# Kernel optimization log

Hardware: AMD Instinct MI355X
Metric: run time of the kernel (lower is better)

Reference implementation:

```python
import jax, jax.numpy as jnp
import numpy as np

B, H = 64, 1024
K_CONV = 4


def setup_inputs() -> dict:
    key = jax.random.key(0)
    ks = jax.random.split(key, 12)

    def lin(k, i, o, w_scale=None, b_init=None):
        k1, k2 = jax.random.split(k)
        w = jax.random.normal(k1, (i, o), jnp.float32) / np.float32(np.sqrt(i))
        if b_init is None:
            b = jnp.zeros((o,), jnp.float32)
        else:
            b = b_init(k2, o)
        return w, b

    Wq, bq = lin(ks[0], H, H)
    Wk, bk = lin(ks[1], H, H)
    Wv, bv = lin(ks[2], H, H)
    # qk_conv: Conv(in_features=1, out_features=1, kernel_size=4) -> kernel (4,1,1), bias (1,)
    conv_w = jax.random.normal(ks[3], (K_CONV, 1, 1), jnp.float32) * 0.5
    conv_b = jnp.zeros((1,), jnp.float32)
    Wi, bi = lin(ks[4], H, 1, b_init=lambda k, o: jax.random.normal(k, (o,), jnp.float32) * 0.01)
    Wf, bf = lin(ks[5], H, 1, b_init=lambda k, o: jax.random.uniform(k, (o,), jnp.float32, 3.0, 6.0))
    Wo, bo = lin(ks[6], H, H)
    Wskip, bskip = lin(ks[7], H, H)

    c = jnp.zeros((B * H * H,), jnp.float32)
    n = jnp.zeros((B * H,), jnp.float32)
    m = jnp.zeros((B,), jnp.float32)
    x = jax.random.normal(ks[8], (B, H), jnp.float32)

    return {
        "c": c, "n": n, "m": m, "x": x,
        "Wq": Wq, "bq": bq, "Wk": Wk, "bk": bk, "Wv": Wv, "bv": bv,
        "conv_w": conv_w, "conv_b": conv_b,
        "Wi": Wi, "bi": bi, "Wf": Wf, "bf": bf,
        "Wo": Wo, "bo": bo, "Wskip": Wskip, "bskip": bskip,
    }


def reference(c, n, m, x, Wq, bq, Wk, bk, Wv, bv, conv_w, conv_b,
              Wi, bi, Wf, bf, Wo, bo, Wskip, bskip):
    cell = c.reshape(-1, H, H)        # (b, h, h)
    norm = n.reshape(-1, H)           # (b, h)

    out = jax.nn.sigmoid(x @ Wo + bo)                 # (b, h)
    i_tilde = jnp.squeeze(x @ Wi + bi, axis=1)        # (b,)
    f_tilde = jnp.squeeze(x @ Wf + bf, axis=1)        # (b,)

    m_new = jnp.maximum(f_tilde + m, i_tilde)
    i_g = jnp.exp(i_tilde - m_new)
    f_g = jnp.exp(f_tilde + m - m_new)

    # depthwise-style 1D conv over feature axis, 1 in / 1 out channel, SAME pad
    qk = jax.lax.conv_general_dilated(
        x[..., None], conv_w, window_strides=(1,), padding='SAME',
        dimension_numbers=('NWC', 'WIO', 'NWC')) + conv_b   # (b, h, 1)
    qk = jax.nn.silu(qk)[..., 0]                            # (b, h)

    key_ = (qk @ Wk + bk) / jnp.sqrt(jnp.float32(H))  # (b, h)
    query = qk @ Wq + bq                              # (b, h)
    value = x @ Wv + bv                               # (b, h)

    # gated outer-product memory update
    c_new = f_g[:, None, None] * cell + i_g[:, None, None] * (value[:, :, None] * key_[:, None, :])
    n_new = f_g[:, None] * norm + i_g[:, None] * key_

    scaler = jnp.abs(jnp.einsum('bi,bi->b', n_new, query))
    scaler = 1.0 / jnp.maximum(scaler, 1.0)
    h = out * (jnp.einsum('bik,bk->bi', c_new, query) * scaler[:, None])
    h = h + qk @ Wskip + bskip

    return (c_new.reshape(-1), n_new.reshape(-1), m_new, h)
```

## Files before the change

### kernel.cpp

```cpp
#include <hip/hip_runtime.h>
#include <cmath>

#define HH 1024
#define BB 64

#define C_ELEMS ((size_t)BB * HH * HH)

typedef float f4 __attribute__((ext_vector_type(4)));

__device__ __forceinline__ float sigm(float v) { return 1.0f / (1.0f + expf(-v)); }

__global__ __launch_bounds__(256) void kA(
    const float* __restrict__ x, const float* __restrict__ m,
    const float* __restrict__ cw, const float* __restrict__ cb,
    const float* __restrict__ Wi, const float* __restrict__ bi,
    const float* __restrict__ Wf, const float* __restrict__ bf,
    float* __restrict__ qk, float* __restrict__ ig,
    float* __restrict__ fg, float* __restrict__ m_out)
{
    int b = blockIdx.x;
    int tid = threadIdx.x;
    const float* xb = x + (size_t)b * HH;
    float w0 = cw[0], w1 = cw[1], w2 = cw[2], w3 = cw[3], cbv = cb[0];
    int j4 = tid * 4;
    float4 xv = *(const float4*)&xb[j4];
    float xm1 = (tid > 0) ? xb[j4 - 1] : 0.f;
    float xp4 = (tid < 255) ? xb[j4 + 4] : 0.f;
    float xp5 = (tid < 255) ? xb[j4 + 5] : 0.f;
    float s0 = cbv + w0 * xm1  + w1 * xv.x + w2 * xv.y + w3 * xv.z;
    float s1 = cbv + w0 * xv.x + w1 * xv.y + w2 * xv.z + w3 * xv.w;
    float s2 = cbv + w0 * xv.y + w1 * xv.z + w2 * xv.w + w3 * xp4;
    float s3 = cbv + w0 * xv.z + w1 * xv.w + w2 * xp4  + w3 * xp5;
    float4 q;
    q.x = s0 * sigm(s0); q.y = s1 * sigm(s1);
    q.z = s2 * sigm(s2); q.w = s3 * sigm(s3);
    *(float4*)&qk[(size_t)b * HH + j4] = q;

    float4 wi4 = *(const float4*)&Wi[j4];
    float4 wf4 = *(const float4*)&Wf[j4];
    float pi = xv.x * wi4.x + xv.y * wi4.y + xv.z * wi4.z + xv.w * wi4.w;
    float pf = xv.x * wf4.x + xv.y * wf4.y + xv.z * wf4.z + xv.w * wf4.w;

    #pragma unroll
    for (int o = 32; o > 0; o >>= 1) {
        pi += __shfl_down(pi, o, 64);
        pf += __shfl_down(pf, o, 64);
    }
    __shared__ float ri[4], rf[4];
    int wid = tid >> 6, lane = tid & 63;
    if (lane == 0) { ri[wid] = pi; rf[wid] = pf; }
    __syncthreads();
    if (tid == 0) {
        float it = ri[0] + ri[1] + ri[2] + ri[3] + bi[0];
        float ft = rf[0] + rf[1] + rf[2] + rf[3] + bf[0];
        float mo = m[b];
        float mn = fmaxf(ft + mo, it);
        m_out[b] = mn;
        ig[b] = expf(it - mn);
        fg[b] = expf(ft + mo - mn);
    }
}

__global__ __launch_bounds__(256) void kB(
    const float* __restrict__ x, const float* __restrict__ qk,
    const float* __restrict__ Wo, const float* __restrict__ Wv,
    const float* __restrict__ Wk, const float* __restrict__ Wq,
    const float* __restrict__ Wsk, float* __restrict__ part)
{
    int jt = blockIdx.x, ks = blockIdx.y, mat = blockIdx.z;
    const float* W; const float* src;
    switch (mat) {
        case 0: W = Wo;  src = x;  break;
        case 1: W = Wv;  src = x;  break;
        case 2: W = Wk;  src = qk; break;
        case 3: W = Wq;  src = qk; break;
        default: W = Wsk; src = qk; break;
    }
    int j0 = jt * 64;
    int i_base = ks * 128;
    int tid = threadIdx.x;
    int jg = tid & 15;
    int bg = tid >> 4;
    int b0 = bg * 4;

    __shared__ float wlds[32 * 64];
    __shared__ float xlds[32 * 68];

    float acc[4][4];
    #pragma unroll
    for (int a = 0; a < 4; ++a)
        #pragma unroll
        for (int d = 0; d < 4; ++d) acc[a][d] = 0.f;

    for (int ch = 0; ch < 4; ++ch) {
        int i0 = i_base + ch * 32;
        {
            int ii = tid >> 4;
            int c4 = (tid & 15) * 4;
            float4 wa = *(const float4*)&W[(size_t)(i0 + ii) * HH + j0 + c4];
            float4 wb = *(const float4*)&W[(size_t)(i0 + ii + 16) * HH + j0 + c4];
            *(float4*)&wlds[ii * 64 + c4] = wa;
            *(float4*)&wlds[(ii + 16) * 64 + c4] = wb;
        }
        {
            int b = tid >> 2;
            int ii0 = (tid & 3) * 8;
            float4 xa = *(const float4*)&src[(size_t)b * HH + i0 + ii0];
            float4 xb = *(const float4*)&src[(size_t)b * HH + i0 + ii0 + 4];
            xlds[(ii0 + 0) * 68 + b] = xa.x;
            xlds[(ii0 + 1) * 68 + b] = xa.y;
            xlds[(ii0 + 2) * 68 + b] = xa.z;
            xlds[(ii0 + 3) * 68 + b] = xa.w;
            xlds[(ii0 + 4) * 68 + b] = xb.x;
            xlds[(ii0 + 5) * 68 + b] = xb.y;
            xlds[(ii0 + 6) * 68 + b] = xb.z;
            xlds[(ii0 + 7) * 68 + b] = xb.w;
        }
        __syncthreads();
        #pragma unroll
        for (int ii = 0; ii < 32; ++ii) {
            float4 wv = *(const float4*)&wlds[ii * 64 + jg * 4];
            float4 xv = *(const float4*)&xlds[ii * 68 + b0];
            acc[0][0] += xv.x * wv.x; acc[0][1] += xv.x * wv.y;
            acc[0][2] += xv.x * wv.z; acc[0][3] += xv.x * wv.w;
            acc[1][0] += xv.y * wv.x; acc[1][1] += xv.y * wv.y;
            acc[1][2] += xv.y * wv.z; acc[1][3] += xv.y * wv.w;
            acc[2][0] += xv.z * wv.x; acc[2][1] += xv.z * wv.y;
            acc[2][2] += xv.z * wv.z; acc[2][3] += xv.z * wv.w;
            acc[3][0] += xv.w * wv.x; acc[3][1] += xv.w * wv.y;
            acc[3][2] += xv.w * wv.z; acc[3][3] += xv.w * wv.w;
        }
        __syncthreads();
    }
    float* p = part + (size_t)(mat * 8 + ks) * (BB * HH);
    #pragma unroll
    for (int a = 0; a < 4; ++a) {
        float4 v = make_float4(acc[a][0], acc[a][1], acc[a][2], acc[a][3]);
        *(float4*)&p[(size_t)(b0 + a) * HH + j0 + jg * 4] = v;
    }
}

__global__ __launch_bounds__(256) void kC(
    const float* __restrict__ part, const float* __restrict__ n_in,
    const float* __restrict__ bo, const float* __restrict__ bv,
    const float* __restrict__ bk, const float* __restrict__ bq,
    const float* __restrict__ bsk,
    const float* __restrict__ ig, const float* __restrict__ fg,
    float* __restrict__ out_s, float* __restrict__ value_s,
    float* __restrict__ key_s, float* __restrict__ query_s,
    float* __restrict__ skip_s, float* __restrict__ dotp,
    float* __restrict__ n_out)
{
    int seg = blockIdx.x, b = blockIdx.y;
    int tid = threadIdx.x;
    int j = seg * 256 + tid;
    size_t base = (size_t)b * HH + j;
    float s0 = 0.f, s1 = 0.f, s2 = 0.f, s3 = 0.f, s4 = 0.f;
    #pragma unroll
    for (int ksp = 0; ksp < 8; ++ksp) {
        size_t o = (size_t)ksp * (BB * HH) + base;
        s0 += part[(size_t)(0 * 8) * (BB * HH) + o];
        s1 += part[(size_t)(1 * 8) * (BB * HH) + o];
        s2 += part[(size_t)(2 * 8) * (BB * HH) + o];
        s3 += part[(size_t)(3 * 8) * (BB * HH) + o];
        s4 += part[(size_t)(4 * 8) * (BB * HH) + o];
    }
    const float rsH = 0.03125f;
    float og = sigm(s0 + bo[j]);
    float vl = s1 + bv[j];
    float ky = (s2 + bk[j]) * rsH;
    float qu = s3 + bq[j];
    float sk = s4 + bsk[j];

    out_s[base]   = og;
    value_s[base] = vl;
    key_s[base]   = ky;
    query_s[base] = qu;
    skip_s[base]  = sk;

    float igv = ig[b], fgv = fg[b];
    float nn = fgv * n_in[base] + igv * ky;
    n_out[base] = nn;

    float d = nn * qu;
    #pragma unroll
    for (int o = 32; o > 0; o >>= 1) d += __shfl_down(d, o, 64);
    __shared__ float red[4];
    int wid = tid >> 6, lane = tid & 63;
    if (lane == 0) red[wid] = d;
    __syncthreads();
    if (tid == 0) dotp[b * 4 + seg] = red[0] + red[1] + red[2] + red[3];
}

__global__ __launch_bounds__(256) void kD(
    const float* __restrict__ c,
    const float* __restrict__ key_s, const float* __restrict__ query_s,
    const float* __restrict__ value_s, const float* __restrict__ out_s,
    const float* __restrict__ skip_s, const float* __restrict__ ig,
    const float* __restrict__ fg, const float* __restrict__ dotp,
    float* __restrict__ c_out, float* __restrict__ h_out)
{
    int wid = threadIdx.x >> 6;
    int lane = threadIdx.x & 63;
    int r = blockIdx.x * 4 + wid;
    int b = r >> 10;
    float fgv = fg[b];
    float iv = ig[b] * value_s[r];
    const f4* crow = (const f4*)(c + ((size_t)r << 10));
    f4* orow = (f4*)(c_out + ((size_t)r << 10));
    const float* keyb = key_s + (size_t)b * HH;
    const float* qb = query_s + (size_t)b * HH;
    float dot = 0.f;
    #pragma unroll
    for (int kk = 0; kk < 4; ++kk) {
        int k4 = kk * 64 + lane;
        f4 c4 = __builtin_nontemporal_load(&crow[k4]);
        float4 kx = *(const float4*)&keyb[k4 * 4];
        float4 q4 = *(const float4*)&qb[k4 * 4];
        f4 cn;
        cn.x = fgv * c4.x + iv * kx.x;
        cn.y = fgv * c4.y + iv * kx.y;
        cn.z = fgv * c4.z + iv * kx.z;
        cn.w = fgv * c4.w + iv * kx.w;
        __builtin_nontemporal_store(cn, &orow[k4]);
        dot += cn.x * q4.x + cn.y * q4.y + cn.z * q4.z + cn.w * q4.w;
    }
    #pragma unroll
    for (int d = 32; d > 0; d >>= 1) dot += __shfl_down(dot, d, 64);
    if (lane == 0) {
        float ds = dotp[b * 4 + 0] + dotp[b * 4 + 1] + dotp[b * 4 + 2] + dotp[b * 4 + 3];
        float scl = 1.0f / fmaxf(fabsf(ds), 1.0f);
        h_out[r] = out_s[r] * dot * scl + skip_s[r];
    }
}

extern "C" void kernel_launch(void* const* d_in, const int* in_sizes, int n_in,
                              void* d_out, int out_size, void* d_ws, size_t ws_size,
                              hipStream_t stream)
{
    const float* c   = (const float*)d_in[0];
    const float* n   = (const float*)d_in[1];
    const float* m   = (const float*)d_in[2];
    const float* x   = (const float*)d_in[3];
    const float* Wq  = (const float*)d_in[4];
    const float* bq  = (const float*)d_in[5];
    const float* Wk  = (const float*)d_in[6];
    const float* bk  = (const float*)d_in[7];
    const float* Wv  = (const float*)d_in[8];
    const float* bv  = (const float*)d_in[9];
    const float* cw  = (const float*)d_in[10];
    const float* cb  = (const float*)d_in[11];
    const float* Wi  = (const float*)d_in[12];
    const float* bi  = (const float*)d_in[13];
    const float* Wf  = (const float*)d_in[14];
    const float* bf  = (const float*)d_in[15];
    const float* Wo  = (const float*)d_in[16];
    const float* bo  = (const float*)d_in[17];
    const float* Wsk = (const float*)d_in[18];
    const float* bsk = (const float*)d_in[19];

    float* out = (float*)d_out;
    float* ws  = (float*)d_ws;

    const int BH = BB * HH;
    float* qk      = ws;
    float* ig      = ws + BH;
    float* fg      = ig + BB;
    float* dotp    = fg + BB;
    float* fin     = dotp + 256;
    float* out_s   = fin + 0 * BH;
    float* value_s = fin + 1 * BH;
    float* key_s   = fin + 2 * BH;
    float* query_s = fin + 3 * BH;
    float* skip_s  = fin + 4 * BH;
    float* part    = fin + 5 * BH;

    float* c_out = out;
    float* n_out = out + C_ELEMS;
    float* m_out = out + C_ELEMS + BH;
    float* h_out = m_out + BB;

    kA<<<BB, 256, 0, stream>>>(x, m, cw, cb, Wi, bi, Wf, bf, qk, ig, fg, m_out);
    dim3 gB(16, 8, 5);
    kB<<<gB, 256, 0, stream>>>(x, qk, Wo, Wv, Wk, Wq, Wsk, part);
    dim3 gC(4, BB);
    kC<<<gC, 256, 0, stream>>>(part, n, bo, bv, bk, bq, bsk, ig, fg,
                               out_s, value_s, key_s, query_s, skip_s, dotp, n_out);
    kD<<<BH / 4, 256, 0, stream>>>(c, key_s, query_s, value_s, out_s, skip_s,
                                   ig, fg, dotp, c_out, h_out);
}
```

Baseline: 477.8 us.

## Fuse split-K reduction epilogue into GEMV kernel via last-block atomic counter

Removes the separate reduction kernel kC by having the last of the 40 blocks that finish each 64-column tile, detected through an atomic counter reset in kA, sum the split-K partials and compute the gates, key, query, value, skip, n_new and per-tile dot partials. Per-batch dot partials are now stored 16 per batch and summed with vector loads in kD. This saves one kernel launch and its scheduling gap, at the cost of threadfence and atomic overhead and a serialized tail in the finishing block of each tile. The dominant cost is still kD streaming the large c matrix, so the saving is small relative to total time.

```diff
diff --git a/kernel.cpp b/kernel.cpp
--- a/kernel.cpp
+++ b/kernel.cpp
@@ -16,10 +16,12 @@
     const float* __restrict__ Wi, const float* __restrict__ bi,
     const float* __restrict__ Wf, const float* __restrict__ bf,
     float* __restrict__ qk, float* __restrict__ ig,
-    float* __restrict__ fg, float* __restrict__ m_out)
+    float* __restrict__ fg, float* __restrict__ m_out,
+    unsigned* __restrict__ cnt)
 {
     int b = blockIdx.x;
     int tid = threadIdx.x;
+    if (b == 0 && tid < 16) cnt[tid] = 0u;
     const float* xb = x + (size_t)b * HH;
     float w0 = cw[0], w1 = cw[1], w2 = cw[2], w3 = cw[3], cbv = cb[0];
     int j4 = tid * 4;
@@ -65,7 +67,16 @@
     const float* __restrict__ x, const float* __restrict__ qk,
     const float* __restrict__ Wo, const float* __restrict__ Wv,
     const float* __restrict__ Wk, const float* __restrict__ Wq,
-    const float* __restrict__ Wsk, float* __restrict__ part)
+    const float* __restrict__ Wsk, float* __restrict__ part,
+    const float* __restrict__ n_in,
+    const float* __restrict__ bo, const float* __restrict__ bv,
+    const float* __restrict__ bk, const float* __restrict__ bq,
+    const float* __restrict__ bsk,
+    const float* __restrict__ ig, const float* __restrict__ fg,
+    float* __restrict__ out_s, float* __restrict__ value_s,
+    float* __restrict__ key_s, float* __restrict__ query_s,
+    float* __restrict__ skip_s, float* __restrict__ dotp,
+    float* __restrict__ n_out, unsigned* __restrict__ cnt)
 {
     int jt = blockIdx.x, ks = blockIdx.y, mat = blockIdx.z;
     const float* W; const float* src;
@@ -85,6 +96,7 @@
 
     __shared__ float wlds[32 * 64];
     __shared__ float xlds[32 * 68];
+    __shared__ unsigned old_s;
 
     float acc[4][4];
     #pragma unroll
@@ -138,58 +150,62 @@
         float4 v = make_float4(acc[a][0], acc[a][1], acc[a][2], acc[a][3]);
         *(float4*)&p[(size_t)(b0 + a) * HH + j0 + jg * 4] = v;
     }
-}
-
-__global__ __launch_bounds__(256) void kC(
-    const float* __restrict__ part, const float* __restrict__ n_in,
-    const float* __restrict__ bo, const float* __restrict__ bv,
-    const float* __restrict__ bk, const float* __restrict__ bq,
-    const float* __restrict__ bsk,
-    const float* __restrict__ ig, const float* __restrict__ fg,
-    float* __restrict__ out_s, float* __restrict__ value_s,
-    float* __restrict__ key_s, float* __restrict__ query_s,
-    float* __restrict__ skip_s, float* __restrict__ dotp,
-    float* __restrict__ n_out)
-{
-    int seg = blockIdx.x, b = blockIdx.y;
-    int tid = threadIdx.x;
-    int j = seg * 256 + tid;
-    size_t base = (size_t)b * HH + j;
-    float s0 = 0.f, s1 = 0.f, s2 = 0.f, s3 = 0.f, s4 = 0.f;
-    #pragma unroll
-    for (int ksp = 0; ksp < 8; ++ksp) {
-        size_t o = (size_t)ksp * (BB * HH) + base;
-        s0 += part[(size_t)(0 * 8) * (BB * HH) + o];
-        s1 += part[(size_t)(1 * 8) * (BB * HH) + o];
-        s2 += part[(size_t)(2 * 8) * (BB * HH) + o];
-        s3 += part[(size_t)(3 * 8) * (BB * HH) + o];
-        s4 += part[(size_t)(4 * 8) * (BB * HH) + o];
-    }
-    const float rsH = 0.03125f;
-    float og = sigm(s0 + bo[j]);
-    float vl = s1 + bv[j];
-    float ky = (s2 + bk[j]) * rsH;
-    float qu = s3 + bq[j];
-    float sk = s4 + bsk[j];
-
-    out_s[base]   = og;
-    value_s[base] = vl;
-    key_s[base]   = ky;
-    query_s[base] = qu;
-    skip_s[base]  = sk;
-
-    float igv = ig[b], fgv = fg[b];
-    float nn = fgv * n_in[base] + igv * ky;
-    n_out[base] = nn;
-
-    float d = nn * qu;
-    #pragma unroll
-    for (int o = 32; o > 0; o >>= 1) d += __shfl_down(d, o, 64);
-    __shared__ float red[4];
-    int wid = tid >> 6, lane = tid & 63;
-    if (lane == 0) red[wid] = d;
+
     __syncthreads();
-    if (tid == 0) dotp[b * 4 + seg] = red[0] + red[1] + red[2] + red[3];
+    if (tid == 0) {
+        __threadfence();
+        old_s = atomicAdd(&cnt[jt], 1u);
+    }
+    __syncthreads();
+    if (old_s == 39u) {
+        __threadfence();
+        int b = tid >> 2;
+        int jj0 = (tid & 3) * 16;
+        size_t base = (size_t)b * HH + j0 + jj0;
+        float igv = ig[b], fgv = fg[b];
+        const float rsH = 0.03125f;
+        float dsum = 0.f;
+        #pragma unroll 1
+        for (int q4i = 0; q4i < 4; ++q4i) {
+            size_t idx = base + q4i * 4;
+            int j = j0 + jj0 + q4i * 4;
+            f4 s0 = {0.f, 0.f, 0.f, 0.f};
+            f4 s1 = s0, s2 = s0, s3 = s0, s4 = s0;
+            #pragma unroll
+            for (int ksp = 0; ksp < 8; ++ksp) {
+                size_t o = (size_t)ksp * (BB * HH) + idx;
+                s0 += *(const f4*)&part[o];
+                s1 += *(const f4*)&part[(size_t)( 8) * (BB * HH) + o];
+                s2 += *(const f4*)&part[(size_t)(16) * (BB * HH) + o];
+                s3 += *(const f4*)&part[(size_t)(24) * (BB * HH) + o];
+                s4 += *(const f4*)&part[(size_t)(32) * (BB * HH) + o];
+            }
+            f4 bo4 = *(const f4*)&bo[j];
+            f4 bv4 = *(const f4*)&bv[j];
+            f4 bk4 = *(const f4*)&bk[j];
+            f4 bq4 = *(const f4*)&bq[j];
+            f4 bs4 = *(const f4*)&bsk[j];
+            f4 og;
+            og.x = sigm(s0.x + bo4.x); og.y = sigm(s0.y + bo4.y);
+            og.z = sigm(s0.z + bo4.z); og.w = sigm(s0.w + bo4.w);
+            f4 vl = s1 + bv4;
+            f4 ky = (s2 + bk4) * rsH;
+            f4 qu = s3 + bq4;
+            f4 sk = s4 + bs4;
+            *(f4*)&out_s[idx]   = og;
+            *(f4*)&value_s[idx] = vl;
+            *(f4*)&key_s[idx]   = ky;
+            *(f4*)&query_s[idx] = qu;
+            *(f4*)&skip_s[idx]  = sk;
+            f4 nv = *(const f4*)&n_in[idx];
+            f4 nn = fgv * nv + igv * ky;
+            *(f4*)&n_out[idx] = nn;
+            dsum += nn.x * qu.x + nn.y * qu.y + nn.z * qu.z + nn.w * qu.w;
+        }
+        dsum += __shfl_down(dsum, 2, 4);
+        dsum += __shfl_down(dsum, 1, 4);
+        if ((tid & 3) == 0) dotp[b * 16 + jt] = dsum;
+    }
 }
 
 __global__ __launch_bounds__(256) void kD(
@@ -228,7 +244,9 @@
     #pragma unroll
     for (int d = 32; d > 0; d >>= 1) dot += __shfl_down(dot, d, 64);
     if (lane == 0) {
-        float ds = dotp[b * 4 + 0] + dotp[b * 4 + 1] + dotp[b * 4 + 2] + dotp[b * 4 + 3];
+        const f4* dp = (const f4*)(dotp + b * 16);
+        f4 a = dp[0] + dp[1] + dp[2] + dp[3];
+        float ds = a.x + a.y + a.z + a.w;
         float scl = 1.0f / fmaxf(fabsf(ds), 1.0f);
         h_out[r] = out_s[r] * dot * scl + skip_s[r];
     }
@@ -267,7 +285,8 @@
     float* ig      = ws + BH;
     float* fg      = ig + BB;
     float* dotp    = fg + BB;
-    float* fin     = dotp + 256;
+    unsigned* cnt  = (unsigned*)(dotp + 1024);
+    float* fin     = (float*)(cnt + 16);
     float* out_s   = fin + 0 * BH;
     float* value_s = fin + 1 * BH;
     float* key_s   = fin + 2 * BH;
@@ -280,12 +299,11 @@
     float* m_out = out + C_ELEMS + BH;
     float* h_out = m_out + BB;
 
-    kA<<<BB, 256, 0, stream>>>(x, m, cw, cb, Wi, bi, Wf, bf, qk, ig, fg, m_out);
+    kA<<<BB, 256, 0, stream>>>(x, m, cw, cb, Wi, bi, Wf, bf, qk, ig, fg, m_out, cnt);
     dim3 gB(16, 8, 5);
-    kB<<<gB, 256, 0, stream>>>(x, qk, Wo, Wv, Wk, Wq, Wsk, part);
-    dim3 gC(4, BB);
-    kC<<<gC, 256, 0, stream>>>(part, n, bo, bv, bk, bq, bsk, ig, fg,
-                               out_s, value_s, key_s, query_s, skip_s, dotp, n_out);
+    kB<<<gB, 256, 0, stream>>>(x, qk, Wo, Wv, Wk, Wq, Wsk, part,
+                               n, bo, bv, bk, bq, bsk, ig, fg,
+                               out_s, value_s, key_s, query_s, skip_s, dotp, n_out, cnt);
     kD<<<BH / 4, 256, 0, stream>>>(c, key_s, query_s, value_s, out_s, skip_s,
                                    ig, fg, dotp, c_out, h_out);
 }
```

Result: slower. 522.4 us (+9.4%).
